# Kernel tuning notes

Measured on AMD Instinct MI355X. Metric: run time of the kernel, lower is better.

The kernel has to match this reference:

```python
import jax, jax.numpy as jnp
import numpy as np

K = 1e-3          # sigmoid temperature from MAPLoss(k=0.001): sigmoid(x) = 1/(1+exp(-x/K))
N, D = 512, 128   # batch of embeddings
NUM_CLASSES = 32
EPS = 1e-8


def setup_inputs() -> dict:
    key = jax.random.key(0)
    k1, k2 = jax.random.split(key)
    return {
        "input": jax.random.normal(k1, (N, D), dtype=jnp.float32),
        "target": jax.random.randint(k2, (N,), 0, NUM_CLASSES, dtype=jnp.int64),
    }


def _offdiag_cols(n):
    # cols[i, j] = j-th column index != i, in increasing order (matches
    # torch sm[~eye].view(n, n-1) row-major off-diagonal extraction)
    idx = jnp.arange(n - 1)[None, :]
    rows = jnp.arange(n)[:, None]
    return idx + (idx >= rows)  # [n, n-1] int


def reference(input, target):
    n = input.shape[0]
    # cosine similarity matrix
    norms = jnp.maximum(jnp.linalg.norm(input, axis=1, keepdims=True), EPS)
    xn = input / norms
    sm = xn @ xn.T  # [n, n]

    cols = _offdiag_cols(n)  # [n, n-1]
    ranking = jnp.take_along_axis(sm, cols, axis=1)  # [n, n-1]
    gt_full = (target[None, :] == target[:, None])    # [n, n] bool
    gt = jnp.take_along_axis(gt_full, cols, axis=1).astype(input.dtype)  # [n, n-1]

    # indicator[i, j, l] = sigmoid((r[i, l] - r[i, j]) / K)   -- O(n^3) cube
    indicator = jax.nn.sigmoid((ranking[:, None, :] - ranking[:, :, None]) / K)

    accumulated_gt = jnp.einsum('il,ijl->ij', gt, indicator)  # [n, n-1]
    denom = indicator.sum(-1) + 0.5                           # [n, n-1]
    prec = accumulated_gt / denom
    ap = jnp.sum(gt * prec, axis=1)    # [n]
    num_positives = gt.sum(-1)         # [n]

    valid = num_positives > 0
    ap_norm = jnp.where(valid, ap / jnp.where(valid, num_positives, 1.0), 0.0)
    n_valid = valid.sum().astype(input.dtype)
    return 1.0 - ap_norm.sum() / n_valid
```

## Files before the change

kernel.cpp:

```cpp
#include <hip/hip_runtime.h>

#define N 512
#define D 128
#define TS 32
#define RS_SCALE 1442.6950408889634f
#define W_INV (1.0f / 18.0f)
#define B_OFF 1530.0f
#define PADV -1600.0f
#define NB 172

static __device__ __forceinline__ float rcp_fast(float x) {
    return __builtin_amdgcn_rcpf(x);
}
static __device__ __forceinline__ float exp2_fast(float x) {
    return __builtin_amdgcn_exp2f(x);
}

__global__ __launch_bounds__(256) void map_sim_kernel(
    const float* __restrict__ x, float* __restrict__ rs,
    int* __restrict__ ticket)
{
    const int bi = blockIdx.x, bj = blockIdx.y, t = threadIdx.x;
    __shared__ float As[TS * D], Bs[TS * D];
    __shared__ float ssA[TS], ssB[TS];
    __shared__ float invA[TS], invB[TS];

    if (bi == 0 && bj == 0 && t == 0) *ticket = 0;

    const int lane = t & 63;
#pragma unroll
    for (int r = 0; r < 4; ++r) {
        int ch = t + 256 * r;
        int row = ch >> 5, c4 = ch & 31;
        int sw = (c4 ^ (row >> 1)) << 2;
        float4 va = *(const float4*)(x + (bi * TS + row) * D + c4 * 4);
        *(float4*)(As + row * D + sw) = va;
        float pa = va.x * va.x + va.y * va.y + va.z * va.z + va.w * va.w;
        float4 vb = *(const float4*)(x + (bj * TS + row) * D + c4 * 4);
        *(float4*)(Bs + row * D + sw) = vb;
        float pb = vb.x * vb.x + vb.y * vb.y + vb.z * vb.z + vb.w * vb.w;
#pragma unroll
        for (int off = 16; off; off >>= 1) {
            pa += __shfl_xor(pa, off);
            pb += __shfl_xor(pb, off);
        }
        if ((lane & 31) == 0) { ssA[row] = pa; ssB[row] = pb; }
    }
    __syncthreads();
    if (t < TS)          invA[t] = rcp_fast(fmaxf(sqrtf(ssA[t]), 1e-8f));
    else if (t < 2 * TS) invB[t - TS] = rcp_fast(fmaxf(sqrtf(ssB[t - TS]), 1e-8f));
    __syncthreads();

    const int tx = t & 15, ty = t >> 4;
    float acc00 = 0.f, acc01 = 0.f, acc10 = 0.f, acc11 = 0.f;
#pragma unroll 4
    for (int k4 = 0; k4 < D / 4; ++k4) {
        float4 a0 = *(const float4*)(As + (2 * ty) * D + ((k4 ^ ty) << 2));
        float4 a1 = *(const float4*)(As + (2 * ty + 1) * D + ((k4 ^ ty) << 2));
        float4 b0 = *(const float4*)(Bs + (2 * tx) * D + ((k4 ^ tx) << 2));
        float4 b1 = *(const float4*)(Bs + (2 * tx + 1) * D + ((k4 ^ tx) << 2));
        acc00 = fmaf(a0.x, b0.x, acc00); acc00 = fmaf(a0.y, b0.y, acc00);
        acc00 = fmaf(a0.z, b0.z, acc00); acc00 = fmaf(a0.w, b0.w, acc00);
        acc01 = fmaf(a0.x, b1.x, acc01); acc01 = fmaf(a0.y, b1.y, acc01);
        acc01 = fmaf(a0.z, b1.z, acc01); acc01 = fmaf(a0.w, b1.w, acc01);
        acc10 = fmaf(a1.x, b0.x, acc10); acc10 = fmaf(a1.y, b0.y, acc10);
        acc10 = fmaf(a1.z, b0.z, acc10); acc10 = fmaf(a1.w, b0.w, acc10);
        acc11 = fmaf(a1.x, b1.x, acc11); acc11 = fmaf(a1.y, b1.y, acc11);
        acc11 = fmaf(a1.z, b1.z, acc11); acc11 = fmaf(a1.w, b1.w, acc11);
    }

    const float sA0 = invA[2 * ty] * RS_SCALE;
    const float sA1 = invA[2 * ty + 1] * RS_SCALE;
    const float sB0 = invB[2 * tx], sB1 = invB[2 * tx + 1];
    const int gr = bi * TS + 2 * ty, gc = bj * TS + 2 * tx;
    *(float2*)(rs + gr * N + gc) =
        make_float2(acc00 * sA0 * sB0, acc01 * sA0 * sB1);
    *(float2*)(rs + (gr + 1) * N + gc) =
        make_float2(acc10 * sA1 * sB0, acc11 * sA1 * sB1);
}

__global__ __launch_bounds__(512) void map_ap_kernel(
    const float* __restrict__ rs, const int* __restrict__ tgt,
    float2* __restrict__ av, int* __restrict__ ticket,
    float* __restrict__ out)
{
    const int i = blockIdx.x, t = threadIdx.x;
    __shared__ int hist[256];
    __shared__ int offs[NB];
    __shared__ int wtot[4];
    __shared__ float2 skv[N];
    __shared__ float red[16];
    __shared__ int amLast;

    if (t < 256) hist[t] = 0;
    if (t < NB) offs[t] = 0;
    const int ti = tgt[i];
    const bool self = (t == i);
    const float val = self ? PADV : rs[i * N + t];
    const int gti = (!self && tgt[t] == ti) ? 1 : 0;
    int q = (int)((val + B_OFF) * W_INV);
    q = max(0, min(NB - 1, q));
    __syncthreads();
    atomicAdd(&hist[q], (1 << 10) | gti);
    __syncthreads();

    int v = (t < 256) ? hist[t] : 0;
    const int lane = t & 63;
#pragma unroll
    for (int off = 1; off < 64; off <<= 1) {
        int u = __shfl_up(v, off);
        if (lane >= off) v += u;
    }
    if (t < 256 && lane == 63) wtot[t >> 6] = v;
    __syncthreads();
    if (t < 256) {
        int w = t >> 6, add = 0;
        if (w > 0) add += wtot[0];
        if (w > 1) add += wtot[1];
        if (w > 2) add += wtot[2];
        hist[t] = v + add;
    }
    __syncthreads();

    {
        int base = (q > 0) ? (hist[q - 1] >> 10) : 0;
        int pos = base + atomicAdd(&offs[q], 1);
        skv[pos] = make_float2(val, (float)gti);
    }
    __syncthreads();

    const float2 me = skv[t];
    const float rj = me.x, gtj = me.y;
    int qj = (int)((rj + B_OFF) * W_INV);
    qj = max(0, min(NB - 1, qj));
    const int lo = (qj > 1) ? (hist[qj - 2] >> 10) : 0;
    const int e1 = min(qj + 1, NB - 1);
    const int hi = hist[e1] >> 10;

    float dsum = (float)(N - hi);
    float gsum = (float)((hist[NB - 1] & 1023) - (hist[e1] & 1023));
    for (int idx = lo; idx < hi; ++idx) {
        float2 kv = skv[idx];
        float s = rcp_fast(1.f + exp2_fast(rj - kv.x));
        dsum += s;
        gsum = fmaf(kv.y, s, gsum);
    }

    float prec = gsum * rcp_fast(dsum + 0.5f);
    float ap = gtj * prec;
    float np = gtj;

#pragma unroll
    for (int off = 32; off; off >>= 1) {
        ap += __shfl_down(ap, off);
        np += __shfl_down(np, off);
    }
    if ((t & 63) == 0) { red[(t >> 6) * 2] = ap; red[(t >> 6) * 2 + 1] = np; }
    __syncthreads();
    if (t == 0) {
        float A = 0.f, P = 0.f;
#pragma unroll
        for (int k = 0; k < 8; ++k) { A += red[2 * k]; P += red[2 * k + 1]; }
        av[i] = make_float2((P > 0.f) ? (A * rcp_fast(P)) : 0.f,
                            (P > 0.f) ? 1.f : 0.f);
        __threadfence();
        int old = atomicAdd(ticket, 1);
        amLast = (old == (int)gridDim.x - 1) ? 1 : 0;
    }
    __syncthreads();

    if (amLast) {
        __threadfence();
        float2 p = av[t];
        float a = p.x, vv = p.y;
#pragma unroll
        for (int off = 32; off; off >>= 1) {
            a += __shfl_down(a, off);
            vv += __shfl_down(vv, off);
        }
        if ((t & 63) == 0) { red[(t >> 6) * 2] = a; red[(t >> 6) * 2 + 1] = vv; }
        __syncthreads();
        if (t == 0) {
            float A = 0.f, V = 0.f;
#pragma unroll
            for (int k = 0; k < 8; ++k) { A += red[2 * k]; V += red[2 * k + 1]; }
            out[0] = 1.0f - A * rcp_fast(V);
        }
    }
}

extern "C" void kernel_launch(void* const* d_in, const int* in_sizes, int n_in,
                              void* d_out, int out_size, void* d_ws, size_t ws_size,
                              hipStream_t stream) {
    const float* x = (const float*)d_in[0];
    const int* tgt = (const int*)d_in[1];
    float* out = (float*)d_out;

    float* rs = (float*)d_ws;
    float2* av = (float2*)((char*)d_ws + N * N * 4);
    int* ticket = (int*)((char*)d_ws + N * N * 4 + N * 8);

    map_sim_kernel<<<dim3(N / TS, N / TS), 256, 0, stream>>>(x, rs, ticket);
    map_ap_kernel<<<N, 512, 0, stream>>>(rs, tgt, av, ticket, out);
}
```

Before: 29.86 us.

## Fuse similarity and AP kernels into one cooperative kernel with grid syncs

Merges the similarity-matrix kernel and the per-row AP kernel into a single cooperative launch of 256 blocks of 512 threads. Grid-wide syncs replace the kernel boundary and the atomic-ticket final reduction. Each block computes one 32x32 similarity tile and then processes two rows of AP. This removes one launch and the ticket atomics, but adds the cost of two grid barriers and halves the row-level parallelism in the AP phase.

```diff
diff --git a/kernel.cpp b/kernel.cpp
--- a/kernel.cpp
+++ b/kernel.cpp
@@ -1,4 +1,7 @@
 #include <hip/hip_runtime.h>
+#include <hip/hip_cooperative_groups.h>
+
+namespace cg = cooperative_groups;
 
 #define N 512
 #define D 128
@@ -16,21 +19,25 @@
     return __builtin_amdgcn_exp2f(x);
 }
 
-__global__ __launch_bounds__(256) void map_sim_kernel(
-    const float* __restrict__ x, float* __restrict__ rs,
-    int* __restrict__ ticket)
+__global__ __launch_bounds__(512) void map_fused_kernel(
+    const float* __restrict__ x, const int* __restrict__ tgt,
+    float* __restrict__ rs, float2* __restrict__ av, float* __restrict__ out)
 {
-    const int bi = blockIdx.x, bj = blockIdx.y, t = threadIdx.x;
+    const int b = blockIdx.x, t = threadIdx.x;
     __shared__ float As[TS * D], Bs[TS * D];
     __shared__ float ssA[TS], ssB[TS];
     __shared__ float invA[TS], invB[TS];
-
-    if (bi == 0 && bj == 0 && t == 0) *ticket = 0;
-
+    __shared__ int hist[256];
+    __shared__ int offs[NB];
+    __shared__ int wtot[4];
+    __shared__ float2 skv[N];
+    __shared__ float red[16];
+
+    const int bi = b >> 4, bj = b & 15;
     const int lane = t & 63;
 #pragma unroll
-    for (int r = 0; r < 4; ++r) {
-        int ch = t + 256 * r;
+    for (int r = 0; r < 2; ++r) {
+        int ch = t + 512 * r;
         int row = ch >> 5, c4 = ch & 31;
         int sw = (c4 ^ (row >> 1)) << 2;
         float4 va = *(const float4*)(x + (bi * TS + row) * D + c4 * 4);
@@ -51,126 +58,115 @@
     else if (t < 2 * TS) invB[t - TS] = rcp_fast(fmaxf(sqrtf(ssB[t - TS]), 1e-8f));
     __syncthreads();
 
-    const int tx = t & 15, ty = t >> 4;
-    float acc00 = 0.f, acc01 = 0.f, acc10 = 0.f, acc11 = 0.f;
+    if (t < 256) {
+        const int tx = t & 15, ty = t >> 4;
+        float acc00 = 0.f, acc01 = 0.f, acc10 = 0.f, acc11 = 0.f;
 #pragma unroll 4
-    for (int k4 = 0; k4 < D / 4; ++k4) {
-        float4 a0 = *(const float4*)(As + (2 * ty) * D + ((k4 ^ ty) << 2));
-        float4 a1 = *(const float4*)(As + (2 * ty + 1) * D + ((k4 ^ ty) << 2));
-        float4 b0 = *(const float4*)(Bs + (2 * tx) * D + ((k4 ^ tx) << 2));
-        float4 b1 = *(const float4*)(Bs + (2 * tx + 1) * D + ((k4 ^ tx) << 2));
-        acc00 = fmaf(a0.x, b0.x, acc00); acc00 = fmaf(a0.y, b0.y, acc00);
-        acc00 = fmaf(a0.z, b0.z, acc00); acc00 = fmaf(a0.w, b0.w, acc00);
-        acc01 = fmaf(a0.x, b1.x, acc01); acc01 = fmaf(a0.y, b1.y, acc01);
-        acc01 = fmaf(a0.z, b1.z, acc01); acc01 = fmaf(a0.w, b1.w, acc01);
-        acc10 = fmaf(a1.x, b0.x, acc10); acc10 = fmaf(a1.y, b0.y, acc10);
-        acc10 = fmaf(a1.z, b0.z, acc10); acc10 = fmaf(a1.w, b0.w, acc10);
-        acc11 = fmaf(a1.x, b1.x, acc11); acc11 = fmaf(a1.y, b1.y, acc11);
-        acc11 = fmaf(a1.z, b1.z, acc11); acc11 = fmaf(a1.w, b1.w, acc11);
-    }
-
-    const float sA0 = invA[2 * ty] * RS_SCALE;
-    const float sA1 = invA[2 * ty + 1] * RS_SCALE;
-    const float sB0 = invB[2 * tx], sB1 = invB[2 * tx + 1];
-    const int gr = bi * TS + 2 * ty, gc = bj * TS + 2 * tx;
-    *(float2*)(rs + gr * N + gc) =
-        make_float2(acc00 * sA0 * sB0, acc01 * sA0 * sB1);
-    *(float2*)(rs + (gr + 1) * N + gc) =
-        make_float2(acc10 * sA1 * sB0, acc11 * sA1 * sB1);
-}
-
-__global__ __launch_bounds__(512) void map_ap_kernel(
-    const float* __restrict__ rs, const int* __restrict__ tgt,
-    float2* __restrict__ av, int* __restrict__ ticket,
-    float* __restrict__ out)
-{
-    const int i = blockIdx.x, t = threadIdx.x;
-    __shared__ int hist[256];
-    __shared__ int offs[NB];
-    __shared__ int wtot[4];
-    __shared__ float2 skv[N];
-    __shared__ float red[16];
-    __shared__ int amLast;
-
-    if (t < 256) hist[t] = 0;
-    if (t < NB) offs[t] = 0;
-    const int ti = tgt[i];
-    const bool self = (t == i);
-    const float val = self ? PADV : rs[i * N + t];
-    const int gti = (!self && tgt[t] == ti) ? 1 : 0;
-    int q = (int)((val + B_OFF) * W_INV);
-    q = max(0, min(NB - 1, q));
-    __syncthreads();
-    atomicAdd(&hist[q], (1 << 10) | gti);
-    __syncthreads();
-
-    int v = (t < 256) ? hist[t] : 0;
-    const int lane = t & 63;
-#pragma unroll
-    for (int off = 1; off < 64; off <<= 1) {
-        int u = __shfl_up(v, off);
-        if (lane >= off) v += u;
-    }
-    if (t < 256 && lane == 63) wtot[t >> 6] = v;
-    __syncthreads();
-    if (t < 256) {
-        int w = t >> 6, add = 0;
-        if (w > 0) add += wtot[0];
-        if (w > 1) add += wtot[1];
-        if (w > 2) add += wtot[2];
-        hist[t] = v + add;
-    }
-    __syncthreads();
-
-    {
-        int base = (q > 0) ? (hist[q - 1] >> 10) : 0;
-        int pos = base + atomicAdd(&offs[q], 1);
-        skv[pos] = make_float2(val, (float)gti);
-    }
-    __syncthreads();
-
-    const float2 me = skv[t];
-    const float rj = me.x, gtj = me.y;
-    int qj = (int)((rj + B_OFF) * W_INV);
-    qj = max(0, min(NB - 1, qj));
-    const int lo = (qj > 1) ? (hist[qj - 2] >> 10) : 0;
-    const int e1 = min(qj + 1, NB - 1);
-    const int hi = hist[e1] >> 10;
-
-    float dsum = (float)(N - hi);
-    float gsum = (float)((hist[NB - 1] & 1023) - (hist[e1] & 1023));
-    for (int idx = lo; idx < hi; ++idx) {
-        float2 kv = skv[idx];
-        float s = rcp_fast(1.f + exp2_fast(rj - kv.x));
-        dsum += s;
-        gsum = fmaf(kv.y, s, gsum);
-    }
-
-    float prec = gsum * rcp_fast(dsum + 0.5f);
-    float ap = gtj * prec;
-    float np = gtj;
-
-#pragma unroll
-    for (int off = 32; off; off >>= 1) {
-        ap += __shfl_down(ap, off);
-        np += __shfl_down(np, off);
-    }
-    if ((t & 63) == 0) { red[(t >> 6) * 2] = ap; red[(t >> 6) * 2 + 1] = np; }
-    __syncthreads();
-    if (t == 0) {
-        float A = 0.f, P = 0.f;
-#pragma unroll
-        for (int k = 0; k < 8; ++k) { A += red[2 * k]; P += red[2 * k + 1]; }
-        av[i] = make_float2((P > 0.f) ? (A * rcp_fast(P)) : 0.f,
-                            (P > 0.f) ? 1.f : 0.f);
-        __threadfence();
-        int old = atomicAdd(ticket, 1);
-        amLast = (old == (int)gridDim.x - 1) ? 1 : 0;
-    }
-    __syncthreads();
-
-    if (amLast) {
-        __threadfence();
+        for (int k4 = 0; k4 < D / 4; ++k4) {
+            float4 a0 = *(const float4*)(As + (2 * ty) * D + ((k4 ^ ty) << 2));
+            float4 a1 = *(const float4*)(As + (2 * ty + 1) * D + ((k4 ^ ty) << 2));
+            float4 b0 = *(const float4*)(Bs + (2 * tx) * D + ((k4 ^ tx) << 2));
+            float4 b1 = *(const float4*)(Bs + (2 * tx + 1) * D + ((k4 ^ tx) << 2));
+            acc00 = fmaf(a0.x, b0.x, acc00); acc00 = fmaf(a0.y, b0.y, acc00);
+            acc00 = fmaf(a0.z, b0.z, acc00); acc00 = fmaf(a0.w, b0.w, acc00);
+            acc01 = fmaf(a0.x, b1.x, acc01); acc01 = fmaf(a0.y, b1.y, acc01);
+            acc01 = fmaf(a0.z, b1.z, acc01); acc01 = fmaf(a0.w, b1.w, acc01);
+            acc10 = fmaf(a1.x, b0.x, acc10); acc10 = fmaf(a1.y, b0.y, acc10);
+            acc10 = fmaf(a1.z, b0.z, acc10); acc10 = fmaf(a1.w, b0.w, acc10);
+            acc11 = fmaf(a1.x, b1.x, acc11); acc11 = fmaf(a1.y, b1.y, acc11);
+            acc11 = fmaf(a1.z, b1.z, acc11); acc11 = fmaf(a1.w, b1.w, acc11);
+        }
+        const float sA0 = invA[2 * ty] * RS_SCALE;
+        const float sA1 = invA[2 * ty + 1] * RS_SCALE;
+        const float sB0 = invB[2 * tx], sB1 = invB[2 * tx + 1];
+        const int gr = bi * TS + 2 * ty, gc = bj * TS + 2 * tx;
+        *(float2*)(rs + gr * N + gc) =
+            make_float2(acc00 * sA0 * sB0, acc01 * sA0 * sB1);
+        *(float2*)(rs + (gr + 1) * N + gc) =
+            make_float2(acc10 * sA1 * sB0, acc11 * sA1 * sB1);
+    }
+
+    cg::this_grid().sync();
+
+    for (int ri = 0; ri < 2; ++ri) {
+        const int i = b + 256 * ri;
+        __syncthreads();
+        if (t < 256) hist[t] = 0;
+        if (t < NB) offs[t] = 0;
+        const int ti = tgt[i];
+        const bool self = (t == i);
+        const float val = self ? PADV : rs[i * N + t];
+        const int gti = (!self && tgt[t] == ti) ? 1 : 0;
+        int q = (int)((val + B_OFF) * W_INV);
+        q = max(0, min(NB - 1, q));
+        __syncthreads();
+        atomicAdd(&hist[q], (1 << 10) | gti);
+        __syncthreads();
+
+        int v = (t < 256) ? hist[t] : 0;
+#pragma unroll
+        for (int off = 1; off < 64; off <<= 1) {
+            int u = __shfl_up(v, off);
+            if (lane >= off) v += u;
+        }
+        if (t < 256 && lane == 63) wtot[t >> 6] = v;
+        __syncthreads();
+        if (t < 256) {
+            int w = t >> 6, add = 0;
+            if (w > 0) add += wtot[0];
+            if (w > 1) add += wtot[1];
+            if (w > 2) add += wtot[2];
+            hist[t] = v + add;
+        }
+        __syncthreads();
+
+        {
+            int base = (q > 0) ? (hist[q - 1] >> 10) : 0;
+            int pos = base + atomicAdd(&offs[q], 1);
+            skv[pos] = make_float2(val, (float)gti);
+        }
+        __syncthreads();
+
+        const float2 me = skv[t];
+        const float rj = me.x, gtj = me.y;
+        int qj = (int)((rj + B_OFF) * W_INV);
+        qj = max(0, min(NB - 1, qj));
+        const int lo = (qj > 1) ? (hist[qj - 2] >> 10) : 0;
+        const int e1 = min(qj + 1, NB - 1);
+        const int hi = hist[e1] >> 10;
+
+        float dsum = (float)(N - hi);
+        float gsum = (float)((hist[NB - 1] & 1023) - (hist[e1] & 1023));
+        for (int idx = lo; idx < hi; ++idx) {
+            float2 kv = skv[idx];
+            float s = rcp_fast(1.f + exp2_fast(rj - kv.x));
+            dsum += s;
+            gsum = fmaf(kv.y, s, gsum);
+        }
+
+        float prec = gsum * rcp_fast(dsum + 0.5f);
+        float ap = gtj * prec;
+        float np = gtj;
+
+#pragma unroll
+        for (int off = 32; off; off >>= 1) {
+            ap += __shfl_down(ap, off);
+            np += __shfl_down(np, off);
+        }
+        if ((t & 63) == 0) { red[(t >> 6) * 2] = ap; red[(t >> 6) * 2 + 1] = np; }
+        __syncthreads();
+        if (t == 0) {
+            float A = 0.f, P = 0.f;
+#pragma unroll
+            for (int k = 0; k < 8; ++k) { A += red[2 * k]; P += red[2 * k + 1]; }
+            av[i] = make_float2((P > 0.f) ? (A * rcp_fast(P)) : 0.f,
+                                (P > 0.f) ? 1.f : 0.f);
+        }
+    }
+
+    cg::this_grid().sync();
+
+    if (b == 0) {
         float2 p = av[t];
         float a = p.x, vv = p.y;
 #pragma unroll
@@ -198,8 +194,8 @@
 
     float* rs = (float*)d_ws;
     float2* av = (float2*)((char*)d_ws + N * N * 4);
-    int* ticket = (int*)((char*)d_ws + N * N * 4 + N * 8);
-
-    map_sim_kernel<<<dim3(N / TS, N / TS), 256, 0, stream>>>(x, rs, ticket);
-    map_ap_kernel<<<N, 512, 0, stream>>>(rs, tgt, av, ticket, out);
-}
+
+    void* args[] = {(void*)&x, (void*)&tgt, (void*)&rs, (void*)&av, (void*)&out};
+    hipLaunchCooperativeKernel((void*)map_fused_kernel, dim3(256), dim3(512),
+                               args, 0, stream);
+}
```

After: 85.32 us. 2.86x slower.

## Halve AP block size, process two ranks per thread with wave-uniform windows

Applied to the files above, without the earlier changes.

The AP kernel now runs 256 threads per row, and each thread handles two candidates for the histogram build and two ranks for the sigmoid window sum. The window bounds are made uniform across the wavefront, taken from the first and last lane's bucket, so loops do not diverge, and the inner loop reads two sorted entries at once through float4 loads. This cuts thread count and divergence, and the code relies on sorted order making the window contiguous. In exchange, each lane may evaluate extra pairs outside its own narrow window, and there is less parallelism per row.

```diff
diff --git a/kernel.cpp b/kernel.cpp
--- a/kernel.cpp
+++ b/kernel.cpp
@@ -79,41 +79,47 @@
         make_float2(acc10 * sA1 * sB0, acc11 * sA1 * sB1);
 }
 
-__global__ __launch_bounds__(512) void map_ap_kernel(
+__global__ __launch_bounds__(256) void map_ap_kernel(
     const float* __restrict__ rs, const int* __restrict__ tgt,
     float2* __restrict__ av, int* __restrict__ ticket,
     float* __restrict__ out)
 {
     const int i = blockIdx.x, t = threadIdx.x;
+    const int lane = t & 63;
     __shared__ int hist[256];
     __shared__ int offs[NB];
     __shared__ int wtot[4];
-    __shared__ float2 skv[N];
-    __shared__ float red[16];
+    __shared__ __align__(16) float2 skv[N];
+    __shared__ float red[8];
     __shared__ int amLast;
 
-    if (t < 256) hist[t] = 0;
+    hist[t] = 0;
     if (t < NB) offs[t] = 0;
     const int ti = tgt[i];
-    const bool self = (t == i);
-    const float val = self ? PADV : rs[i * N + t];
-    const int gti = (!self && tgt[t] == ti) ? 1 : 0;
-    int q = (int)((val + B_OFF) * W_INV);
-    q = max(0, min(NB - 1, q));
-    __syncthreads();
-    atomicAdd(&hist[q], (1 << 10) | gti);
-    __syncthreads();
-
-    int v = (t < 256) ? hist[t] : 0;
-    const int lane = t & 63;
+    float val[2]; int gti[2], q[2];
+#pragma unroll
+    for (int e = 0; e < 2; ++e) {
+        int c = t + 256 * e;
+        bool self = (c == i);
+        val[e] = self ? PADV : rs[i * N + c];
+        gti[e] = (!self && tgt[c] == ti) ? 1 : 0;
+        int qq = (int)((val[e] + B_OFF) * W_INV);
+        q[e] = max(0, min(NB - 1, qq));
+    }
+    __syncthreads();
+    atomicAdd(&hist[q[0]], (1 << 10) | gti[0]);
+    atomicAdd(&hist[q[1]], (1 << 10) | gti[1]);
+    __syncthreads();
+
+    int v = hist[t];
 #pragma unroll
     for (int off = 1; off < 64; off <<= 1) {
         int u = __shfl_up(v, off);
         if (lane >= off) v += u;
     }
-    if (t < 256 && lane == 63) wtot[t >> 6] = v;
-    __syncthreads();
-    if (t < 256) {
+    if (lane == 63) wtot[t >> 6] = v;
+    __syncthreads();
+    {
         int w = t >> 6, add = 0;
         if (w > 0) add += wtot[0];
         if (w > 1) add += wtot[1];
@@ -122,45 +128,62 @@
     }
     __syncthreads();
 
-    {
-        int base = (q > 0) ? (hist[q - 1] >> 10) : 0;
-        int pos = base + atomicAdd(&offs[q], 1);
-        skv[pos] = make_float2(val, (float)gti);
-    }
-    __syncthreads();
-
-    const float2 me = skv[t];
-    const float rj = me.x, gtj = me.y;
-    int qj = (int)((rj + B_OFF) * W_INV);
-    qj = max(0, min(NB - 1, qj));
-    const int lo = (qj > 1) ? (hist[qj - 2] >> 10) : 0;
-    const int e1 = min(qj + 1, NB - 1);
-    const int hi = hist[e1] >> 10;
-
-    float dsum = (float)(N - hi);
-    float gsum = (float)((hist[NB - 1] & 1023) - (hist[e1] & 1023));
-    for (int idx = lo; idx < hi; ++idx) {
-        float2 kv = skv[idx];
-        float s = rcp_fast(1.f + exp2_fast(rj - kv.x));
-        dsum += s;
-        gsum = fmaf(kv.y, s, gsum);
-    }
-
-    float prec = gsum * rcp_fast(dsum + 0.5f);
-    float ap = gtj * prec;
-    float np = gtj;
+#pragma unroll
+    for (int e = 0; e < 2; ++e) {
+        int base = (q[e] > 0) ? (hist[q[e] - 1] >> 10) : 0;
+        int pos = base + atomicAdd(&offs[q[e]], 1);
+        skv[pos] = make_float2(val[e], (float)gti[e]);
+    }
+    __syncthreads();
+
+    const int totGt = hist[NB - 1] & 1023;
+    const float4* skv4 = (const float4*)skv;
+
+    float apAcc = 0.f, npAcc = 0.f;
+#pragma unroll
+    for (int ri = 0; ri < 2; ++ri) {
+        const int p = t + 256 * ri;
+        const float2 me = skv[p];
+        const float rj = me.x, gtj = me.y;
+        int qj = (int)((rj + B_OFF) * W_INV);
+        qj = max(0, min(NB - 1, qj));
+        const int qlo = __shfl(qj, 0);
+        const int qhi = __shfl(qj, 63);
+        const int lo = (qlo > 1) ? (hist[qlo - 2] >> 10) : 0;
+        const int e1 = min(qhi + 1, NB - 1);
+        const int hi = hist[e1] >> 10;
+
+        float dsum = (float)(N - hi);
+        float gsum = (float)(totGt - (hist[e1] & 1023));
+        int k = lo & ~1;
+        for (; k + 2 <= hi; k += 2) {
+            float4 kv = skv4[k >> 1];
+            float s0 = rcp_fast(1.f + exp2_fast(rj - kv.x));
+            float s1 = rcp_fast(1.f + exp2_fast(rj - kv.z));
+            dsum += s0 + s1;
+            gsum = fmaf(kv.y, s0, gsum);
+            gsum = fmaf(kv.w, s1, gsum);
+        }
+        if (k < hi) {
+            float2 kv = skv[k];
+            float s = rcp_fast(1.f + exp2_fast(rj - kv.x));
+            dsum += s;
+            gsum = fmaf(kv.y, s, gsum);
+        }
+        apAcc += gtj * gsum * rcp_fast(dsum + 0.5f);
+        npAcc += gtj;
+    }
 
 #pragma unroll
     for (int off = 32; off; off >>= 1) {
-        ap += __shfl_down(ap, off);
-        np += __shfl_down(np, off);
-    }
-    if ((t & 63) == 0) { red[(t >> 6) * 2] = ap; red[(t >> 6) * 2 + 1] = np; }
+        apAcc += __shfl_down(apAcc, off);
+        npAcc += __shfl_down(npAcc, off);
+    }
+    if (lane == 0) { red[(t >> 6) * 2] = apAcc; red[(t >> 6) * 2 + 1] = npAcc; }
     __syncthreads();
     if (t == 0) {
-        float A = 0.f, P = 0.f;
-#pragma unroll
-        for (int k = 0; k < 8; ++k) { A += red[2 * k]; P += red[2 * k + 1]; }
+        float A = red[0] + red[2] + red[4] + red[6];
+        float P = red[1] + red[3] + red[5] + red[7];
         av[i] = make_float2((P > 0.f) ? (A * rcp_fast(P)) : 0.f,
                             (P > 0.f) ? 1.f : 0.f);
         __threadfence();
@@ -171,19 +194,18 @@
 
     if (amLast) {
         __threadfence();
-        float2 p = av[t];
-        float a = p.x, vv = p.y;
+        float2 p0 = av[t], p1 = av[t + 256];
+        float a = p0.x + p1.x, vv = p0.y + p1.y;
 #pragma unroll
         for (int off = 32; off; off >>= 1) {
             a += __shfl_down(a, off);
             vv += __shfl_down(vv, off);
         }
-        if ((t & 63) == 0) { red[(t >> 6) * 2] = a; red[(t >> 6) * 2 + 1] = vv; }
+        if (lane == 0) { red[(t >> 6) * 2] = a; red[(t >> 6) * 2 + 1] = vv; }
         __syncthreads();
         if (t == 0) {
-            float A = 0.f, V = 0.f;
-#pragma unroll
-            for (int k = 0; k < 8; ++k) { A += red[2 * k]; V += red[2 * k + 1]; }
+            float A = red[0] + red[2] + red[4] + red[6];
+            float V = red[1] + red[3] + red[5] + red[7];
             out[0] = 1.0f - A * rcp_fast(V);
         }
     }
@@ -201,5 +223,5 @@
     int* ticket = (int*)((char*)d_ws + N * N * 4 + N * 8);
 
     map_sim_kernel<<<dim3(N / TS, N / TS), 256, 0, stream>>>(x, rs, ticket);
-    map_ap_kernel<<<N, 512, 0, stream>>>(rs, tgt, av, ticket, out);
-}
+    map_ap_kernel<<<N, 256, 0, stream>>>(rs, tgt, av, ticket, out);
+}
```

New measurement: 33.01 us. 10.5% more time.
